# Performance work log

Hardware: AMD Instinct MI355X
Metric: run time of the kernel (lower is better)

## Reference

```python
import jax, jax.numpy as jnp
import numpy as np

H_DIM = 128
RES_H = 64
N_RES = 2
N_E = 1024
E_DIM = 64
BETA = 0.25


def conv2d(x, w, stride, padding):
    return jax.lax.conv_general_dilated(
        x, w, (stride, stride), padding,
        dimension_numbers=('NCHW', 'OIHW', 'NCHW'))


def setup_inputs() -> dict:
    key = jax.random.key(0)
    ks = jax.random.split(key, 8)
    def winit(k, shape, fan_in):
        return jax.random.normal(k, shape, jnp.float32) * (1.0 / np.sqrt(fan_in))
    x = jax.random.normal(ks[0], (8, 3, 512, 512), jnp.float32)
    conv1_w = winit(ks[1], (H_DIM // 2, 3, 4, 4), 3 * 16)
    conv1_b = jnp.zeros((H_DIM // 2,), jnp.float32)
    conv2_w = winit(ks[2], (H_DIM, H_DIM // 2, 4, 4), (H_DIM // 2) * 16)
    conv2_b = jnp.zeros((H_DIM,), jnp.float32)
    # ResidualStack shares ONE ResidualLayer's weights across n_res_layers (ModuleList([layer]*n))
    res_w1 = winit(ks[3], (RES_H, H_DIM, 3, 3), H_DIM * 9)   # 3x3, pad 1, no bias
    res_w2 = winit(ks[4], (H_DIM, RES_H, 1, 1), RES_H)       # 1x1, no bias
    preq_w = winit(ks[5], (E_DIM, H_DIM, 1, 1), H_DIM)
    preq_b = jnp.zeros((E_DIM,), jnp.float32)
    # torch code fills codebook with 1.0 (degenerate); use random codebook for a meaningful baseline
    emb = jax.random.normal(ks[6], (N_E, E_DIM), jnp.float32) * 0.5
    return dict(x=x, conv1_w=conv1_w, conv1_b=conv1_b, conv2_w=conv2_w,
                conv2_b=conv2_b, res_w1=res_w1, res_w2=res_w2,
                preq_w=preq_w, preq_b=preq_b, emb=emb)


def reference(x, conv1_w, conv1_b, conv2_w, conv2_b, res_w1, res_w2, preq_w, preq_b, emb):
    # ----- Encoder -----
    h = jax.nn.relu(conv2d(x, conv1_w, 4, 'VALID') + conv1_b[None, :, None, None])
    h = conv2d(h, conv2_w, 4, 'VALID') + conv2_b[None, :, None, None]
    for _ in range(N_RES):  # shared weights, applied N_RES times
        r = conv2d(jax.nn.relu(h), res_w1, 1, 'SAME')
        r = conv2d(jax.nn.relu(r), res_w2, 1, 'VALID')
        h = h + r
    h = jax.nn.relu(h)
    # ----- pre-quantization 1x1 conv -----
    z_e = conv2d(h, preq_w, 1, 'VALID') + preq_b[None, :, None, None]  # [B,E,32,32]
    # ----- Vector quantization -----
    z = jnp.transpose(z_e, (0, 2, 3, 1))              # [B,32,32,E]
    zf = z.reshape(-1, E_DIM)                         # [N,E], N = B*32*32
    d = (jnp.sum(zf * zf, axis=1, keepdims=True)
         + jnp.sum(emb * emb, axis=1)
         - 2.0 * (zf @ emb.T))                        # [N, n_e]
    idx = jnp.argmin(d, axis=1)                       # [N]
    one_hot = jax.nn.one_hot(idx, N_E, dtype=zf.dtype)  # [N, n_e]
    z_q1 = (one_hot @ emb).reshape(z.shape)           # quantized latents
    sg = jax.lax.stop_gradient
    loss = jnp.mean((z_q1 - z) ** 2) + BETA * jnp.mean((z_q1 - sg(z)) ** 2)
    z_q = z + (z_q1 - sg(z))                          # straight-through
    e_mean = jnp.mean(one_hot, axis=0)
    perplexity = jnp.exp(-jnp.sum(e_mean * jnp.log(e_mean + 1e-10)))
    z_q = jnp.transpose(z_q, (0, 3, 1, 2))            # [B,E,32,32]
    return (loss, z_q, perplexity, emb, idx[:, None])
```

## Files before the change

kernel.cpp:

```cpp
#include <hip/hip_runtime.h>

#define NPOS 8192
#define ZQ_OFF   1
#define PPL_OFF  524289
#define EMB_OFF  524290
#define IDX_OFF  589826

__global__ __launch_bounds__(256) void k_conv1(const float* __restrict__ x,
    const float* __restrict__ w, const float* __restrict__ bias,
    float* __restrict__ out) {
  __shared__ float A[48*64];
  __shared__ float B[48*64];
  const int b = blockIdx.z, oy = blockIdx.y, xh = blockIdx.x;
  const int tid = threadIdx.x, lane = tid & 63;
  const int wv = __builtin_amdgcn_readfirstlane(tid >> 6);
  const int col = lane & 31, og = lane >> 5;
  const float* xb = x + (size_t)b*786432 + (size_t)(oy*4)*512 + xh*256;
#pragma unroll
  for (int j = 0; j < 3; ++j) {
    int f = tid + j*256;
    int c = f >> 8, iy = (f >> 6) & 3, x4 = f & 63;
    float4 v = *(const float4*)(xb + (size_t)c*262144 + (size_t)iy*512 + x4*4);
    int k0 = c*16 + iy*4;
    A[(k0+0)*64 + x4] = v.x;
    A[(k0+1)*64 + x4] = v.y;
    A[(k0+2)*64 + x4] = v.z;
    A[(k0+3)*64 + x4] = v.w;
  }
#pragma unroll
  for (int j = 0; j < 3; ++j) {
    int fi = tid + j*256;
    float4 v = ((const float4*)w)[fi];
    int base = fi*4;
#pragma unroll
    for (int e = 0; e < 4; ++e) {
      int f = base + e;
      int oc = f / 48, k = f - oc*48;
      B[k*64 + oc] = (&v.x)[e];
    }
  }
  __syncthreads();
  const int ocb = wv*16 + og*8;
  float acc0[8], acc1[8];
#pragma unroll
  for (int j = 0; j < 8; ++j) { acc0[j] = bias[ocb+j]; acc1[j] = acc0[j]; }
  const float* ap = A + col;
  const float* bp = B + ocb;
#pragma unroll 8
  for (int k = 0; k < 48; ++k) {
    float a0 = ap[k*64];
    float a1 = ap[k*64 + 32];
    float4 b0 = *(const float4*)(bp + k*64);
    float4 b1 = *(const float4*)(bp + k*64 + 4);
    acc0[0] += a0*b0.x; acc0[1] += a0*b0.y; acc0[2] += a0*b0.z; acc0[3] += a0*b0.w;
    acc0[4] += a0*b1.x; acc0[5] += a0*b1.y; acc0[6] += a0*b1.z; acc0[7] += a0*b1.w;
    acc1[0] += a1*b0.x; acc1[1] += a1*b0.y; acc1[2] += a1*b0.z; acc1[3] += a1*b0.w;
    acc1[4] += a1*b1.x; acc1[5] += a1*b1.y; acc1[6] += a1*b1.z; acc1[7] += a1*b1.w;
  }
  float* ob = out + ((size_t)(b*64 + ocb))*16384 + oy*128 + xh*64 + col;
#pragma unroll
  for (int j = 0; j < 8; ++j) {
    ob[(size_t)j*16384]      = fmaxf(acc0[j], 0.f);
    ob[(size_t)j*16384 + 32] = fmaxf(acc1[j], 0.f);
  }
}

__global__ __launch_bounds__(256) void k_conv2p(const float* __restrict__ h1,
    const float* __restrict__ w, float* __restrict__ pd) {
  __shared__ float Asm[128*64];
  __shared__ float Bsm[128*64];
  const int b = blockIdx.z, pg = blockIdx.y;
  const int kc = blockIdx.x & 1, ocg = blockIdx.x >> 1;
  const int tid = threadIdx.x;
  const int lane = tid & 63;
  const int wv = __builtin_amdgcn_readfirstlane(tid >> 6);
  const int ox = lane & 31, og = lane >> 5;
  float4 pa[8], pb[8];
  const float* srcA = h1 + ((size_t)(b*64 + kc*32)) * 16384 + (size_t)(pg*8) * 128;
  const float* srcB = w + (size_t)(ocg*64) * 1024 + kc*512;
#define C2P_LOAD(t) { \
    _Pragma("unroll") \
    for (int j = 0; j < 8; ++j) { \
      int f = tid + j*256; \
      int x4 = f & 31, r = (f>>5) & 7, i = f >> 8; \
      pa[j] = *(const float4*)(srcA + (size_t)((t)*8+i)*16384 + r*128 + x4*4); \
      int oc = f & 63, kq = f >> 6; \
      pb[j] = *(const float4*)(srcB + (size_t)oc*1024 + (t)*128 + kq*4); \
    } }
  C2P_LOAD(0)
  float acc0[8] = {0,0,0,0,0,0,0,0};
  float acc1[8] = {0,0,0,0,0,0,0,0};
  const float* ap = &Asm[ox];
  const float* bp = &Bsm[wv*16 + og*8];
  for (int t = 0; t < 4; ++t) {
    __syncthreads();
#pragma unroll
    for (int j = 0; j < 8; ++j) {
      int f = tid + j*256;
      int x4 = f & 31, r = (f>>5) & 7, i = f >> 8;
      int k0 = i*16 + (r&3)*4, pos = (r>>2)*32 + x4;
      Asm[(k0+0)*64+pos] = pa[j].x;
      Asm[(k0+1)*64+pos] = pa[j].y;
      Asm[(k0+2)*64+pos] = pa[j].z;
      Asm[(k0+3)*64+pos] = pa[j].w;
      int oc = f & 63, kq = f >> 6;
      Bsm[(kq*4+0)*64+oc] = pb[j].x;
      Bsm[(kq*4+1)*64+oc] = pb[j].y;
      Bsm[(kq*4+2)*64+oc] = pb[j].z;
      Bsm[(kq*4+3)*64+oc] = pb[j].w;
    }
    __syncthreads();
    if (t < 3) C2P_LOAD(t+1)
#pragma unroll 8
    for (int k = 0; k < 128; ++k) {
      float a0 = ap[k*64];
      float a1 = ap[k*64+32];
      float4 b0 = *(const float4*)&bp[k*64];
      float4 b1 = *(const float4*)&bp[k*64+4];
      acc0[0] += a0*b0.x; acc0[1] += a0*b0.y; acc0[2] += a0*b0.z; acc0[3] += a0*b0.w;
      acc0[4] += a0*b1.x; acc0[5] += a0*b1.y; acc0[6] += a0*b1.z; acc0[7] += a0*b1.w;
      acc1[0] += a1*b0.x; acc1[1] += a1*b0.y; acc1[2] += a1*b0.z; acc1[3] += a1*b0.w;
      acc1[4] += a1*b1.x; acc1[5] += a1*b1.y; acc1[6] += a1*b1.z; acc1[7] += a1*b1.w;
    }
  }
  const int ocb = ocg*64 + wv*16 + og*8;
  float* o0 = pd + (size_t)kc*1048576 + ((size_t)b*128 + ocb)*1024 + (pg*2)*32 + ox;
  float* o1 = o0 + 32;
#pragma unroll
  for (int j = 0; j < 8; ++j) {
    o0[(size_t)j*1024] = acc0[j];
    o1[(size_t)j*1024] = acc1[j];
  }
}

__global__ __launch_bounds__(256) void k_c2red(const float* __restrict__ pd,
    const float* __restrict__ bias, float* __restrict__ h) {
  int i4 = blockIdx.x*256 + threadIdx.x;
  int oc = (i4 >> 8) & 127;
  float bv = bias[oc];
  const float4 p0 = ((const float4*)pd)[i4];
  const float4 p1 = ((const float4*)pd)[i4 + 262144];
  float4 r;
  r.x = bv + p0.x + p1.x; r.y = bv + p0.y + p1.y;
  r.z = bv + p0.z + p1.z; r.w = bv + p0.w + p1.w;
  ((float4*)h)[i4] = r;
}

__global__ __launch_bounds__(256) void k_res3(const float* __restrict__ h,
    const float* __restrict__ w, float* __restrict__ pd3) {
  __shared__ float A[72*64];
  __shared__ float B[72*64];
  const int b = blockIdx.z, yp = blockIdx.y, kc = blockIdx.x;
  const int tid = threadIdx.x, lane = tid & 63;
  const int wv = __builtin_amdgcn_readfirstlane(tid >> 6);
  const int col = lane & 31, og = lane >> 5;
  const int prow = lane >> 5;
  const float* hb = h + (size_t)b*131072;
  const int row0 = yp*2;
  float acc0[8] = {0,0,0,0,0,0,0,0};
  float acc1[8] = {0,0,0,0,0,0,0,0};
  for (int tt = 0; tt < 4; ++tt) {
    const int ic0 = kc*32 + tt*8;
    __syncthreads();
#pragma unroll
    for (int j = 0; j < 18; ++j) {
      int k_rel = wv + j*4;
      int ic_r = k_rel / 9;
      int tap = k_rel - ic_r*9;
      int dy = tap / 3, dx = tap - dy*3;
      int py = row0 + prow + dy - 1;
      int px = col + dx - 1;
      float v = 0.f;
      if (((unsigned)py < 32u) && ((unsigned)px < 32u))
        v = fmaxf(hb[(size_t)(ic0+ic_r)*1024 + py*32 + px], 0.f);
      A[k_rel*64 + lane] = v;
    }
#pragma unroll
    for (int j = 0; j < 5; ++j) {
      int fi = tid + j*256;
      if (fi < 1152) {
        int oc = fi / 18, r = fi - oc*18;
        float4 v = *(const float4*)(w + (size_t)oc*1152 + ic0*9 + r*4);
        int kb = r*4;
        B[(kb+0)*64 + oc] = v.x;
        B[(kb+1)*64 + oc] = v.y;
        B[(kb+2)*64 + oc] = v.z;
        B[(kb+3)*64 + oc] = v.w;
      }
    }
    __syncthreads();
    const float* ap = A + col;
    const float* bp = B + wv*16 + og*8;
#pragma unroll 8
    for (int k = 0; k < 72; ++k) {
      float a0 = ap[k*64];
      float a1 = ap[k*64 + 32];
      float4 b0 = *(const float4*)(bp + k*64);
      float4 b1 = *(const float4*)(bp + k*64 + 4);
      acc0[0] += a0*b0.x; acc0[1] += a0*b0.y; acc0[2] += a0*b0.z; acc0[3] += a0*b0.w;
      acc0[4] += a0*b1.x; acc0[5] += a0*b1.y; acc0[6] += a0*b1.z; acc0[7] += a0*b1.w;
      acc1[0] += a1*b0.x; acc1[1] += a1*b0.y; acc1[2] += a1*b0.z; acc1[3] += a1*b0.w;
      acc1[4] += a1*b1.x; acc1[5] += a1*b1.y; acc1[6] += a1*b1.z; acc1[7] += a1*b1.w;
    }
  }
  const int ocb = wv*16 + og*8;
  float* o0 = pd3 + (size_t)kc*524288 + ((size_t)b*64 + ocb)*1024 + row0*32 + col;
#pragma unroll
  for (int j = 0; j < 8; ++j) {
    o0[(size_t)j*1024]      = acc0[j];
    o0[(size_t)j*1024 + 32] = acc1[j];
  }
}

__global__ __launch_bounds__(256) void k_r3red(const float* __restrict__ pd3,
    float* __restrict__ r1) {
  int i4 = blockIdx.x*256 + threadIdx.x;
  float4 a = ((const float4*)pd3)[i4];
  float4 b = ((const float4*)pd3)[i4 + 131072];
  float4 c = ((const float4*)pd3)[i4 + 262144];
  float4 d = ((const float4*)pd3)[i4 + 393216];
  float4 r;
  r.x = ((a.x + b.x) + c.x) + d.x;
  r.y = ((a.y + b.y) + c.y) + d.y;
  r.z = ((a.z + b.z) + c.z) + d.z;
  r.w = ((a.w + b.w) + c.w) + d.w;
  ((float4*)r1)[i4] = r;
}

__global__ __launch_bounds__(256) void k_res1(const float* __restrict__ r1,
    const float* __restrict__ w, float* __restrict__ h) {
  __shared__ float B[64*8];
  const int og = blockIdx.y;
  const int tid = threadIdx.x;
#pragma unroll
  for (int j = 0; j < 2; ++j) {
    int f = tid + j*256;
    int ocj = f >> 6, ic = f & 63;
    B[ic*8 + ocj] = w[(size_t)(og*8 + ocj)*64 + ic];
  }
  __syncthreads();
  const int p = blockIdx.x*256 + tid;
  const int b = p >> 10, rem = p & 1023;
  const float* rb = r1 + (size_t)b*65536 + rem;
  float acc[8] = {0,0,0,0,0,0,0,0};
  for (int ic = 0; ic < 64; ++ic) {
    float rv = fmaxf(rb[(size_t)ic*1024], 0.f);
    float4 w0 = *(const float4*)&B[ic*8];
    float4 w1 = *(const float4*)&B[ic*8 + 4];
    acc[0] += w0.x*rv; acc[1] += w0.y*rv; acc[2] += w0.z*rv; acc[3] += w0.w*rv;
    acc[4] += w1.x*rv; acc[5] += w1.y*rv; acc[6] += w1.z*rv; acc[7] += w1.w*rv;
  }
  float* hb = h + ((size_t)b*128 + og*8)*1024 + rem;
#pragma unroll
  for (int j = 0; j < 8; ++j) hb[(size_t)j*1024] += acc[j];
}

__global__ __launch_bounds__(256) void k_preq(const float* __restrict__ h,
    const float* __restrict__ w, const float* __restrict__ bias,
    float* __restrict__ ze) {
  __shared__ float B[128*4];
  const int eg = blockIdx.y;
  const int tid = threadIdx.x;
#pragma unroll
  for (int j = 0; j < 2; ++j) {
    int f = tid + j*256;
    int ej = f >> 7, ic = f & 127;
    B[ic*4 + ej] = w[(size_t)(eg*4 + ej)*128 + ic];
  }
  __syncthreads();
  const int p = blockIdx.x*256 + tid;
  const int b = p >> 10, rem = p & 1023;
  const float* hb = h + (size_t)b*131072 + rem;
  float acc[4] = {0,0,0,0};
  for (int ic = 0; ic < 128; ++ic) {
    float hv = fmaxf(hb[(size_t)ic*1024], 0.f);
    float4 wv4 = *(const float4*)&B[ic*4];
    acc[0] += wv4.x*hv; acc[1] += wv4.y*hv; acc[2] += wv4.z*hv; acc[3] += wv4.w*hv;
  }
#pragma unroll
  for (int j = 0; j < 4; ++j)
    ze[((size_t)b*64 + eg*4+j)*1024 + rem] = acc[j] + bias[eg*4+j];
}

__global__ __launch_bounds__(256) void k_e2(const float* __restrict__ emb,
                                            float* __restrict__ e2) {
  int e = blockIdx.x*256 + threadIdx.x;
  const float* er = emb + (size_t)e*64;
  float s = 0.f;
#pragma unroll
  for (int i = 0; i < 16; ++i) {
    float4 v = *(const float4*)(er + i*4);
    s += v.x*v.x + v.y*v.y + v.z*v.z + v.w*v.w;
  }
  e2[e] = s;
}

__global__ __launch_bounds__(256) void k_vq(const float* __restrict__ ze,
    const float* __restrict__ emb, const float* __restrict__ e2,
    float* __restrict__ part_d, int* __restrict__ part_i) {
  const int bid = blockIdx.x;
  const int sg = bid & 15, pg = bid >> 4;
  const int tid = threadIdx.x, lane = tid & 63;
  const int wv = __builtin_amdgcn_readfirstlane(tid >> 6);
  const int s = sg*4 + wv;
  const int p = pg*64 + lane;
  const int b = p >> 10, rem = p & 1023;
  const float* zb = ze + (size_t)b*64*1024 + rem;
  float z[64];
#pragma unroll
  for (int i = 0; i < 64; ++i) z[i] = zb[(size_t)i*1024];
  float best = 3.4e38f; int bi = 0;
  const float* es = emb + (size_t)s*16*64;
  for (int j4 = 0; j4 < 16; j4 += 4) {
    float a0 = 0.f, a1 = 0.f, a2 = 0.f, a3 = 0.f;
#pragma unroll
    for (int i = 0; i < 64; ++i) {
      float zi = z[i];
      a0 += es[(j4+0)*64+i]*zi;
      a1 += es[(j4+1)*64+i]*zi;
      a2 += es[(j4+2)*64+i]*zi;
      a3 += es[(j4+3)*64+i]*zi;
    }
    float d0 = e2[s*16+j4+0] - 2.f*a0;
    float d1 = e2[s*16+j4+1] - 2.f*a1;
    float d2 = e2[s*16+j4+2] - 2.f*a2;
    float d3 = e2[s*16+j4+3] - 2.f*a3;
    if (d0 < best) { best = d0; bi = s*16+j4+0; }
    if (d1 < best) { best = d1; bi = s*16+j4+1; }
    if (d2 < best) { best = d2; bi = s*16+j4+2; }
    if (d3 < best) { best = d3; bi = s*16+j4+3; }
  }
  part_d[(size_t)s*NPOS + p] = best;
  part_i[(size_t)s*NPOS + p] = bi;
}

__global__ __launch_bounds__(256) void k_reduce(const float* __restrict__ part_d,
    const int* __restrict__ part_i, const float* __restrict__ emb,
    const float* __restrict__ ze, float* __restrict__ out,
    int* __restrict__ counts, float* __restrict__ sse) {
  const int p = blockIdx.x*256 + threadIdx.x;
  float best = 3.4e38f; int id = 0;
  for (int s = 0; s < 64; ++s) {
    float d = part_d[(size_t)s*NPOS + p];
    int   i = part_i[(size_t)s*NPOS + p];
    if (d < best) { best = d; id = i; }
  }
  out[IDX_OFF + p] = (float)id;
  atomicAdd(&counts[id], 1);
  const int b = p >> 10, rem = p & 1023;
  const float* zb = ze + (size_t)b*64*1024 + rem;
  float* qo = out + ZQ_OFF + (size_t)b*64*1024 + rem;
  const float* er = emb + (size_t)id*64;
  float local = 0.f;
#pragma unroll
  for (int e4 = 0; e4 < 16; ++e4) {
    float4 q = *(const float4*)(er + e4*4);
    float z0 = zb[(size_t)(e4*4+0)*1024];
    float z1 = zb[(size_t)(e4*4+1)*1024];
    float z2 = zb[(size_t)(e4*4+2)*1024];
    float z3 = zb[(size_t)(e4*4+3)*1024];
    qo[(size_t)(e4*4+0)*1024] = q.x;
    qo[(size_t)(e4*4+1)*1024] = q.y;
    qo[(size_t)(e4*4+2)*1024] = q.z;
    qo[(size_t)(e4*4+3)*1024] = q.w;
    float d0 = q.x - z0, d1 = q.y - z1, d2 = q.z - z2, d3 = q.w - z3;
    local += d0*d0 + d1*d1 + d2*d2 + d3*d3;
  }
  for (int off = 32; off; off >>= 1) local += __shfl_down(local, off);
  if ((threadIdx.x & 63) == 0) atomicAdd(sse, local);
}

__global__ __launch_bounds__(256) void k_final(const int* __restrict__ counts,
    const float* __restrict__ sse, float* __restrict__ out) {
  __shared__ float red[4];
  float part = 0.f;
  for (int e = threadIdx.x; e < 1024; e += 256) {
    float pm = (float)counts[e] * (1.f/8192.f);
    part += pm * logf(pm + 1e-10f);
  }
  for (int off = 32; off; off >>= 1) part += __shfl_down(part, off);
  if ((threadIdx.x & 63) == 0) red[threadIdx.x >> 6] = part;
  __syncthreads();
  if (threadIdx.x == 0) {
    float t = red[0] + red[1] + red[2] + red[3];
    out[PPL_OFF] = expf(-t);
    out[0] = 1.25f * sse[0] * (1.f/524288.f);
  }
}

extern "C" void kernel_launch(void* const* d_in, const int* in_sizes, int n_in,
                              void* d_out, int out_size, void* d_ws, size_t ws_size,
                              hipStream_t stream) {
  (void)in_sizes; (void)n_in; (void)out_size; (void)ws_size;
  const float* x   = (const float*)d_in[0];
  const float* w1  = (const float*)d_in[1];
  const float* b1  = (const float*)d_in[2];
  const float* w2  = (const float*)d_in[3];
  const float* b2  = (const float*)d_in[4];
  const float* rw1 = (const float*)d_in[5];
  const float* rw2 = (const float*)d_in[6];
  const float* pw  = (const float*)d_in[7];
  const float* pb  = (const float*)d_in[8];
  const float* emb = (const float*)d_in[9];
  float* out = (float*)d_out;
  char* ws = (char*)d_ws;
  float* h1     = (float*)(ws);
  float* pd3    = (float*)(ws);
  float* c2pd   = (float*)(ws + 33554432);
  float* r1     = (float*)(ws + 33554432);
  float* ze     = (float*)(ws + 35651584);
  float* pd     = (float*)(ws + 37748736);
  int*   pi     = (int*)  (ws + 39845888);
  float* h      = (float*)(ws + 41943040);
  float* e2     = (float*)(ws + 46137344);
  int*   counts = (int*)  (ws + 46141440);
  float* sse    = (float*)(ws + 46145536);

  hipMemsetAsync(counts, 0, 1024*4 + 4, stream);
  k_conv1<<<dim3(2,128,8), 256, 0, stream>>>(x, w1, b1, h1);
  k_conv2p<<<dim3(4,16,8), 256, 0, stream>>>(h1, w2, c2pd);
  k_c2red<<<1024, 256, 0, stream>>>(c2pd, b2, h);
  for (int it = 0; it < 2; ++it) {
    k_res3<<<dim3(4,16,8), 256, 0, stream>>>(h, rw1, pd3);
    k_r3red<<<512, 256, 0, stream>>>(pd3, r1);
    k_res1<<<dim3(32,16), 256, 0, stream>>>(r1, rw2, h);
  }
  k_preq<<<dim3(32,16), 256, 0, stream>>>(h, pw, pb, ze);
  k_e2<<<4, 256, 0, stream>>>(emb, e2);
  k_vq<<<2048, 256, 0, stream>>>(ze, emb, e2, pd, pi);
  k_reduce<<<32, 256, 0, stream>>>(pd, pi, emb, ze, out, counts, sse);
  k_final<<<1, 256, 0, stream>>>(counts, sse, out);
  hipMemcpyAsync(out + EMB_OFF, emb, 65536*4, hipMemcpyDeviceToDevice, stream);
}
```

Baseline: 341.5 us.

## Double the split-K factor in res3 and prefetch next chunk into registers

The 3x3 residual conv now splits input channels 8 ways instead of 4, each block processing two 8-channel chunks, which doubles the grid size for more parallelism. The next chunk's activations and weights are prefetched into registers while the current chunk is computed, and weight loads are re-indexed so each lane stores its own output channel without the scatter. The cost is twice as many partial-sum buffers to write and reduce, and the reduction kernel now sums eight slices instead of four.

```diff
diff --git a/kernel.cpp b/kernel.cpp
--- a/kernel.cpp
+++ b/kernel.cpp
@@ -157,38 +157,49 @@
   const int prow = lane >> 5;
   const float* hb = h + (size_t)b*131072;
   const int row0 = yp*2;
+  float prA[18];
+  float4 prB[5];
+#define R3_LOADA(t) { \
+    _Pragma("unroll") \
+    for (int j = 0; j < 18; ++j) { \
+      int k_rel = wv + j*4; \
+      int ic_r = k_rel/9, tap = k_rel - ic_r*9; \
+      int dy = tap/3, dx = tap - dy*3; \
+      int py = row0 + prow + dy - 1, px = col + dx - 1; \
+      float v = 0.f; \
+      if (((unsigned)py < 32u) && ((unsigned)px < 32u)) \
+        v = fmaxf(hb[(size_t)(kc*16 + (t)*8 + ic_r)*1024 + py*32 + px], 0.f); \
+      prA[j] = v; \
+    } }
+#define R3_LOADB(t) { \
+    _Pragma("unroll") \
+    for (int j = 0; j < 5; ++j) { \
+      int rr = wv + j*4; \
+      if (rr < 18) \
+        prB[j] = *(const float4*)(w + (size_t)lane*1152 + (kc*16 + (t)*8)*9 + rr*4); \
+    } }
+  R3_LOADA(0) R3_LOADB(0)
   float acc0[8] = {0,0,0,0,0,0,0,0};
   float acc1[8] = {0,0,0,0,0,0,0,0};
-  for (int tt = 0; tt < 4; ++tt) {
-    const int ic0 = kc*32 + tt*8;
+  for (int tt = 0; tt < 2; ++tt) {
     __syncthreads();
 #pragma unroll
     for (int j = 0; j < 18; ++j) {
       int k_rel = wv + j*4;
-      int ic_r = k_rel / 9;
-      int tap = k_rel - ic_r*9;
-      int dy = tap / 3, dx = tap - dy*3;
-      int py = row0 + prow + dy - 1;
-      int px = col + dx - 1;
-      float v = 0.f;
-      if (((unsigned)py < 32u) && ((unsigned)px < 32u))
-        v = fmaxf(hb[(size_t)(ic0+ic_r)*1024 + py*32 + px], 0.f);
-      A[k_rel*64 + lane] = v;
+      A[k_rel*64 + lane] = prA[j];
     }
 #pragma unroll
     for (int j = 0; j < 5; ++j) {
-      int fi = tid + j*256;
-      if (fi < 1152) {
-        int oc = fi / 18, r = fi - oc*18;
-        float4 v = *(const float4*)(w + (size_t)oc*1152 + ic0*9 + r*4);
-        int kb = r*4;
-        B[(kb+0)*64 + oc] = v.x;
-        B[(kb+1)*64 + oc] = v.y;
-        B[(kb+2)*64 + oc] = v.z;
-        B[(kb+3)*64 + oc] = v.w;
+      int rr = wv + j*4;
+      if (rr < 18) {
+        B[(rr*4+0)*64 + lane] = prB[j].x;
+        B[(rr*4+1)*64 + lane] = prB[j].y;
+        B[(rr*4+2)*64 + lane] = prB[j].z;
+        B[(rr*4+3)*64 + lane] = prB[j].w;
       }
     }
     __syncthreads();
+    if (tt == 0) { R3_LOADA(1) R3_LOADB(1) }
     const float* ap = A + col;
     const float* bp = B + wv*16 + og*8;
 #pragma unroll 8
@@ -215,16 +226,13 @@
 __global__ __launch_bounds__(256) void k_r3red(const float* __restrict__ pd3,
     float* __restrict__ r1) {
   int i4 = blockIdx.x*256 + threadIdx.x;
-  float4 a = ((const float4*)pd3)[i4];
-  float4 b = ((const float4*)pd3)[i4 + 131072];
-  float4 c = ((const float4*)pd3)[i4 + 262144];
-  float4 d = ((const float4*)pd3)[i4 + 393216];
-  float4 r;
-  r.x = ((a.x + b.x) + c.x) + d.x;
-  r.y = ((a.y + b.y) + c.y) + d.y;
-  r.z = ((a.z + b.z) + c.z) + d.z;
-  r.w = ((a.w + b.w) + c.w) + d.w;
-  ((float4*)r1)[i4] = r;
+  float4 s = ((const float4*)pd3)[i4];
+#pragma unroll
+  for (int c = 1; c < 8; ++c) {
+    float4 p = ((const float4*)pd3)[i4 + c*131072];
+    s.x += p.x; s.y += p.y; s.z += p.z; s.w += p.w;
+  }
+  ((float4*)r1)[i4] = s;
 }
 
 __global__ __launch_bounds__(256) void k_res1(const float* __restrict__ r1,
@@ -421,7 +429,7 @@
   k_conv2p<<<dim3(4,16,8), 256, 0, stream>>>(h1, w2, c2pd);
   k_c2red<<<1024, 256, 0, stream>>>(c2pd, b2, h);
   for (int it = 0; it < 2; ++it) {
-    k_res3<<<dim3(4,16,8), 256, 0, stream>>>(h, rw1, pd3);
+    k_res3<<<dim3(8,16,8), 256, 0, stream>>>(h, rw1, pd3);
     k_r3red<<<512, 256, 0, stream>>>(pd3, r1);
     k_res1<<<dim3(32,16), 256, 0, stream>>>(r1, rw2, h);
   }
```

Result: faster. 302.0 us (-11.6%).
